# Performance work log

Measured on AMD Instinct MI355X. Metric: run time of the kernel, lower is better.

Reference implementation:

```python
import jax, jax.numpy as jnp
import numpy as np

NUM_NODES = 100000
NUM_RELS = 500
DIM = 64          # input_dim == hidden_dim == output_dim
NUM_EDGES = 1_000_000
LEAKY_SLOPE = 0.01  # torch F.leaky_relu default


def _linear_params(key, fin, fout):
    # torch nn.Linear default init: U(-1/sqrt(fin), 1/sqrt(fin))
    kw, kb = jax.random.split(key)
    s = 1.0 / np.sqrt(fin)
    W = jax.random.uniform(kw, (fout, fin), minval=-s, maxval=s, dtype=jnp.float32)
    b = jax.random.uniform(kb, (fout,), minval=-s, maxval=s, dtype=jnp.float32)
    return W, b


def setup_inputs() -> dict:
    key = jax.random.key(0)
    ks = jax.random.split(key, 12)
    src_idx = jax.random.randint(ks[0], (NUM_EDGES,), 0, NUM_NODES, dtype=jnp.int32)
    dst_idx = jax.random.randint(ks[1], (NUM_EDGES,), 0, NUM_NODES, dtype=jnp.int32)
    rel_idx = jax.random.randint(ks[2], (NUM_EDGES,), 0, NUM_RELS, dtype=jnp.int32)
    ent_embed = jax.random.normal(ks[3], (NUM_NODES, DIM), dtype=jnp.float32)
    rel_embed = jax.random.normal(ks[4], (NUM_RELS, DIM), dtype=jnp.float32)
    W_ent, b_ent = _linear_params(ks[5], DIM, DIM)          # fc_ent
    W_relL, b_relL = _linear_params(ks[6], DIM, DIM)        # fc_rel
    W_rel2, b_rel2 = _linear_params(ks[7], DIM, DIM)        # fc_rel2
    W_rel3, b_rel3 = _linear_params(ks[8], 3 * DIM, DIM)    # fc_rel3
    W_a, b_a = _linear_params(ks[9], DIM, 1)                # a
    W_fc, b_fc = _linear_params(ks[10], 3 * DIM, DIM)       # fc
    return {
        "ent_embed": ent_embed, "rel_embed": rel_embed,
        "W_ent": W_ent, "b_ent": b_ent,
        "W_relL": W_relL, "b_relL": b_relL,
        "W_rel2": W_rel2, "b_rel2": b_rel2,
        "W_rel3": W_rel3, "b_rel3": b_rel3,
        "W_a": W_a, "b_a": b_a,
        "W_fc": W_fc, "b_fc": b_fc,
        "src_idx": src_idx, "dst_idx": dst_idx, "rel_idx": rel_idx,
    }


def reference(ent_embed, rel_embed, W_ent, b_ent, W_relL, b_relL,
              W_rel2, b_rel2, W_rel3, b_rel3, W_a, b_a, W_fc, b_fc,
              src_idx, dst_idx, rel_idx):
    # --- per-edge projections (first=True path: lookup from learned tables) ---
    src = ent_embed[src_idx] @ W_ent.T + b_ent            # [E, D]
    dst = ent_embed[dst_idx] @ W_ent.T + b_ent            # [E, D]
    rel = rel_embed[rel_idx] @ W_relL.T + b_relL          # [E, D]

    # --- edge message c and unnormalized attention b ---
    c = jnp.concatenate([src, dst, rel], axis=1) @ W_fc.T + b_fc   # [E, D]
    logits = jax.nn.leaky_relu((c @ W_a.T + b_a)[:, 0], LEAKY_SLOPE)  # [E]
    b = jnp.exp(logits)                                    # [E] (original uses plain exp)

    # --- scatter-softmax over edges grouped by source node ---
    b_sum = jax.ops.segment_sum(b, src_idx, num_segments=NUM_NODES)  # [N]
    alpha = b / b_sum[src_idx]                             # [E]

    # --- attention-weighted neighbor aggregation ---
    h_ent = jax.ops.segment_sum(alpha[:, None] * c, src_idx,
                                num_segments=NUM_NODES)    # [N, D]

    # --- relation pooling: mean over edges of each relation ---
    rel2 = rel @ W_rel2.T + b_rel2                         # [E, D]
    feats = jnp.concatenate([h_ent[src_idx], h_ent[dst_idx], rel2], axis=1)  # [E, 3D]
    sums = jax.ops.segment_sum(feats, rel_idx, num_segments=NUM_RELS)        # [R, 3D]
    counts = jax.ops.segment_sum(jnp.ones_like(b), rel_idx, num_segments=NUM_RELS)
    mean = sums / jnp.maximum(counts, 1.0)[:, None]        # [R, 3D]

    h_rel = mean @ W_rel3.T + b_rel3                       # [R, D]
    return (h_ent, h_rel)
```

## Files before the change

kernel.cpp:

```cpp
#include <hip/hip_runtime.h>
#include <hip/hip_fp16.h>
#include <math.h>

#define N_NODES 100000
#define N_RELS  500
#define DIM     64
#define N_EDGES 1000000
#define SLOPE   0.01f
#define RSUB    4
#define SC_EDGES 2048
#define NB_E    489
#define NBKT    196
#define BSH     9
#define NROWS   (N_RELS + NBKT)
#define BMAX    5632

__device__ __forceinline__ unsigned short f2bf(float f) {
    unsigned int u = __float_as_uint(f);
    u += 0x7FFFu + ((u >> 16) & 1u);
    return (unsigned short)(u >> 16);
}
__device__ __forceinline__ float bfl(unsigned int u) { return __uint_as_float(u << 16); }
__device__ __forceinline__ float bfh(unsigned int u) { return __uint_as_float(u & 0xFFFF0000u); }

__device__ __forceinline__ unsigned int f2e5m2(float f) {
    __half h = __float2half_rn(f);
    unsigned short hu;
    __builtin_memcpy(&hu, &h, 2);
    unsigned int u = hu;
    u += 0x7Fu + ((u >> 8) & 1u);
    return (u >> 8) & 0xFFu;
}
__device__ __forceinline__ float e5d(unsigned int b) {
    unsigned short u = (unsigned short)(b << 8);
    __half h;
    __builtin_memcpy(&h, &u, 2);
    return __half2float(h);
}
__device__ __forceinline__ void acc8(float* a, unsigned int x, unsigned int y) {
    a[0] += e5d(x & 255u);         a[1] += e5d((x >> 8) & 255u);
    a[2] += e5d((x >> 16) & 255u); a[3] += e5d(x >> 24);
    a[4] += e5d(y & 255u);         a[5] += e5d((y >> 8) & 255u);
    a[6] += e5d((y >> 16) & 255u); a[7] += e5d(y >> 24);
}
__device__ __forceinline__ void acc16(float* a, uint4 w) {
    acc8(a, w.x, w.y);
    acc8(a + 8, w.z, w.w);
}
__device__ __forceinline__ void accvw(float* a, float b, uint4 vv, uint4 ww) {
    a[0] += b * (bfl(vv.x) + bfl(ww.x));
    a[1] += b * (bfh(vv.x) + bfh(ww.x));
    a[2] += b * (bfl(vv.y) + bfl(ww.y));
    a[3] += b * (bfh(vv.y) + bfh(ww.y));
    a[4] += b * (bfl(vv.z) + bfl(ww.z));
    a[5] += b * (bfh(vv.z) + bfh(ww.z));
    a[6] += b * (bfl(vv.w) + bfl(ww.w));
    a[7] += b * (bfh(vv.w) + bfh(ww.w));
}

__global__ void k_fold(const float* __restrict__ W_ent, const float* __restrict__ b_ent,
                       const float* __restrict__ W_relL, const float* __restrict__ b_relL,
                       const float* __restrict__ W_rel2, const float* __restrict__ b_rel2,
                       const float* __restrict__ W_fc, const float* __restrict__ b_fc,
                       float* __restrict__ Wcat, float* __restrict__ dcat,
                       float* __restrict__ MW, float* __restrict__ MQ,
                       float* __restrict__ dW, float* __restrict__ dQ) {
    int idx = blockIdx.x * 256 + threadIdx.x;
    if (idx < 8192) {
        int k = idx >> 7;
        int j2 = idx & 127;
        int jj = j2 & 63;
        int off = (j2 >> 6) * 64;
        float s = 0.f;
        for (int i = 0; i < 64; i++) s += W_fc[jj*192 + off + i] * W_ent[i*64 + k];
        Wcat[k*128 + j2] = s;
    } else if (idx < 12288) {
        int rem = idx - 8192;
        int j = rem >> 6, i = rem & 63;
        float s = 0.f;
        for (int k = 0; k < 64; k++) s += W_fc[j*192 + 128 + k] * W_relL[k*64 + i];
        MW[j*64 + i] = s;
    } else if (idx < 16384) {
        int rem = idx - 12288;
        int j = rem >> 6, i = rem & 63;
        float s = 0.f;
        for (int k = 0; k < 64; k++) s += W_rel2[j*64 + k] * W_relL[k*64 + i];
        MQ[j*64 + i] = s;
    } else if (idx < 16512) {
        int j2 = idx - 16384;
        int jj = j2 & 63;
        int off = (j2 >> 6) * 64;
        float s = 0.f;
        for (int i = 0; i < 64; i++) s += b_ent[i] * W_fc[jj*192 + off + i];
        dcat[j2] = s;
    } else if (idx < 16640) {
        int rem = idx - 16512;
        int vec = rem >> 6, j = rem & 63;
        if (vec == 0) {
            float s = b_fc[j];
            for (int k = 0; k < 64; k++) s += b_relL[k] * W_fc[j*192 + 128 + k];
            dW[j] = s;
        } else {
            float s = b_rel2[j];
            for (int k = 0; k < 64; k++) s += b_relL[k] * W_rel2[j*64 + k];
            dQ[j] = s;
        }
    }
}

__global__ __launch_bounds__(256) void k_node(const float* __restrict__ ent,
        const float* __restrict__ Wcat, const float* __restrict__ dcat,
        const float* __restrict__ W_a,
        float* __restrict__ Uout, unsigned short* __restrict__ V16,
        float* __restrict__ us, float* __restrict__ vs) {
    __shared__ float sA[64][68];
    __shared__ float sW[64][128];
    int t = threadIdx.x;
    int tile0 = blockIdx.x * 64;
    for (int i = t; i < 2048; i += 256)
        ((float4*)sW)[i] = ((const float4*)Wcat)[i];
    for (int f = t; f < 1024; f += 256) {
        int n = f >> 4, k4 = f & 15;
        float4 v4 = (tile0 + n < N_NODES)
            ? ((const float4*)(ent + (size_t)(tile0 + n) * 64))[k4]
            : make_float4(0.f, 0.f, 0.f, 0.f);
        *(float4*)&sA[n][k4 * 4] = v4;
    }
    __syncthreads();

    int ng = t >> 4;
    int jg = t & 15;
    int n0 = ng * 4;
    int j0 = jg * 8;

    float4 d0 = *(const float4*)(dcat + j0);
    float4 d1 = *(const float4*)(dcat + j0 + 4);
    float acc[4][8];
    #pragma unroll
    for (int a = 0; a < 4; a++) {
        acc[a][0] = d0.x; acc[a][1] = d0.y; acc[a][2] = d0.z; acc[a][3] = d0.w;
        acc[a][4] = d1.x; acc[a][5] = d1.y; acc[a][6] = d1.z; acc[a][7] = d1.w;
    }

    #pragma unroll 4
    for (int k = 0; k < 64; k++) {
        float4 w0 = *(const float4*)&sW[k][j0];
        float4 w1 = *(const float4*)&sW[k][j0 + 4];
        float e0 = sA[n0][k], e1 = sA[n0+1][k], e2 = sA[n0+2][k], e3 = sA[n0+3][k];
        float e[4] = {e0, e1, e2, e3};
        #pragma unroll
        for (int a = 0; a < 4; a++) {
            acc[a][0] += e[a] * w0.x; acc[a][1] += e[a] * w0.y;
            acc[a][2] += e[a] * w0.z; acc[a][3] += e[a] * w0.w;
            acc[a][4] += e[a] * w1.x; acc[a][5] += e[a] * w1.y;
            acc[a][6] += e[a] * w1.z; acc[a][7] += e[a] * w1.w;
        }
    }

    int jw = j0 & 63;
    float4 wa0 = *(const float4*)(W_a + jw);
    float4 wa1 = *(const float4*)(W_a + jw + 4);
    float part[4];
    #pragma unroll
    for (int a = 0; a < 4; a++) {
        part[a] = acc[a][0]*wa0.x + acc[a][1]*wa0.y + acc[a][2]*wa0.z + acc[a][3]*wa0.w
                + acc[a][4]*wa1.x + acc[a][5]*wa1.y + acc[a][6]*wa1.z + acc[a][7]*wa1.w;
    }
    #pragma unroll
    for (int m = 1; m <= 4; m <<= 1) {
        #pragma unroll
        for (int a = 0; a < 4; a++) part[a] += __shfl_xor(part[a], m, 64);
    }
    if ((jg & 7) == 0) {
        float* sv = (jg < 8) ? us : vs;
        #pragma unroll
        for (int a = 0; a < 4; a++)
            if (tile0 + n0 + a < N_NODES) sv[tile0 + n0 + a] = part[a];
    }

    #pragma unroll
    for (int a = 0; a < 4; a++) {
        int n = tile0 + n0 + a;
        if (n >= N_NODES) break;
        if (jg < 8) {
            float4 o0 = make_float4(acc[a][0], acc[a][1], acc[a][2], acc[a][3]);
            float4 o1 = make_float4(acc[a][4], acc[a][5], acc[a][6], acc[a][7]);
            float* base = Uout + (size_t)n * 64 + j0;
            *(float4*)(base) = o0;
            *(float4*)(base + 4) = o1;
        } else {
            uint4 pv;
            pv.x = (unsigned int)f2bf(acc[a][0]) | ((unsigned int)f2bf(acc[a][1]) << 16);
            pv.y = (unsigned int)f2bf(acc[a][2]) | ((unsigned int)f2bf(acc[a][3]) << 16);
            pv.z = (unsigned int)f2bf(acc[a][4]) | ((unsigned int)f2bf(acc[a][5]) << 16);
            pv.w = (unsigned int)f2bf(acc[a][6]) | ((unsigned int)f2bf(acc[a][7]) << 16);
            *(uint4*)(V16 + (size_t)n * 64 + (j0 - 64)) = pv;
        }
    }
}

__global__ __launch_bounds__(256, 2) void k_relproj(const float* __restrict__ relE,
        const float* __restrict__ MW, const float* __restrict__ MQ,
        const float* __restrict__ dW, const float* __restrict__ dQ,
        const float* __restrict__ W_a,
        unsigned short* __restrict__ Wr16, float* __restrict__ Qr, float* __restrict__ wsr) {
    int lane = threadIdx.x & 63;
    int wv = threadIdx.x >> 6;
    float mw[64], mq[64];
    #pragma unroll
    for (int i = 0; i < 64; i++) { mw[i] = MW[lane*64 + i]; mq[i] = MQ[lane*64 + i]; }
    float dw = dW[lane], dq = dQ[lane], wa = W_a[lane];
    int r = blockIdx.x * 4 + wv;
    if (r >= N_RELS) return;
    float e = relE[(size_t)r * 64 + lane];
    float w = dw, q = dq;
    #pragma unroll
    for (int i = 0; i < 64; i++) {
        float ei = __shfl(e, i, 64);
        w += ei * mw[i];
        q += ei * mq[i];
    }
    Wr16[(size_t)r * 64 + lane] = f2bf(w);
    Qr[(size_t)r * 64 + lane] = q;
    float tw = w * wa;
    #pragma unroll
    for (int o = 32; o; o >>= 1) tw += __shfl_xor(tw, o, 64);
    if (lane == 0) wsr[r] = tw;
}

__global__ void k_zero(int* __restrict__ a, int n) {
    int g = blockIdx.x * 256 + threadIdx.x;
    if (g < n) a[g] = 0;
}

__global__ __launch_bounds__(256) void k_hist(const int* __restrict__ src, const int* __restrict__ rel,
        int* __restrict__ cnt_rel, int* __restrict__ bucket_cnt, int* __restrict__ blkhist) {
    __shared__ int lcntR[N_RELS];
    __shared__ int lcntS[NBKT];
    int t = threadIdx.x;
    for (int r = t; r < N_RELS; r += 256) lcntR[r] = 0;
    for (int b = t; b < NBKT; b += 256) lcntS[b] = 0;
    __syncthreads();
    int base = blockIdx.x * SC_EDGES;
    if (base + SC_EDGES <= N_EDGES) {
        int e0 = base + t * 8;
        int4 sa = *(const int4*)(src + e0);
        int4 sb = *(const int4*)(src + e0 + 4);
        int4 ra = *(const int4*)(rel + e0);
        int4 rb = *(const int4*)(rel + e0 + 4);
        atomicAdd(&lcntS[sa.x >> BSH], 1); atomicAdd(&lcntS[sa.y >> BSH], 1);
        atomicAdd(&lcntS[sa.z >> BSH], 1); atomicAdd(&lcntS[sa.w >> BSH], 1);
        atomicAdd(&lcntS[sb.x >> BSH], 1); atomicAdd(&lcntS[sb.y >> BSH], 1);
        atomicAdd(&lcntS[sb.z >> BSH], 1); atomicAdd(&lcntS[sb.w >> BSH], 1);
        atomicAdd(&lcntR[ra.x], 1); atomicAdd(&lcntR[ra.y], 1);
        atomicAdd(&lcntR[ra.z], 1); atomicAdd(&lcntR[ra.w], 1);
        atomicAdd(&lcntR[rb.x], 1); atomicAdd(&lcntR[rb.y], 1);
        atomicAdd(&lcntR[rb.z], 1); atomicAdd(&lcntR[rb.w], 1);
    } else {
        for (int g = base + t; g < N_EDGES; g += 256) {
            atomicAdd(&lcntS[src[g] >> BSH], 1);
            atomicAdd(&lcntR[rel[g]], 1);
        }
    }
    __syncthreads();
    for (int r = t; r < N_RELS; r += 256) {
        int c = lcntR[r];
        blkhist[(size_t)r * NB_E + blockIdx.x] = c;
        if (c) atomicAdd(&cnt_rel[r], c);
    }
    for (int b = t; b < NBKT; b += 256) {
        int c = lcntS[b];
        blkhist[(size_t)(N_RELS + b) * NB_E + blockIdx.x] = c;
        if (c) atomicAdd(&bucket_cnt[b], c);
    }
}

__global__ void k_scan_two(const int* __restrict__ cnt_rel, const int* __restrict__ bucket_cnt,
                           int* __restrict__ starts) {
    __shared__ int tot[256];
    int t = threadIdx.x;
    const int* cnt = blockIdx.x ? bucket_cnt : cnt_rel;
    int n = blockIdx.x ? NBKT : N_RELS;
    int* out = starts + (blockIdx.x ? N_RELS : 0);
    int myv[4];
    int mySum = 0;
    for (int q = 0; q < 4; q++) {
        int g = t * 4 + q;
        int v = (g < n) ? cnt[g] : 0;
        myv[q] = v; mySum += v;
    }
    tot[t] = mySum;
    __syncthreads();
    for (int o = 1; o < 256; o <<= 1) {
        int u = (t >= o) ? tot[t - o] : 0;
        __syncthreads();
        tot[t] += u;
        __syncthreads();
    }
    int run = tot[t] - mySum;
    for (int q = 0; q < 4; q++) {
        int g = t * 4 + q;
        if (g < n) out[g] = run;
        run += myv[q];
    }
}

__global__ __launch_bounds__(256) void k_scan_relblk(const int* __restrict__ starts,
        const int* __restrict__ blkhist, int* __restrict__ blkbase) {
    int lane = threadIdx.x & 63;
    int row = (blockIdx.x * 256 + threadIdx.x) >> 6;
    if (row >= NROWS) return;
    int run = starts[row];
    for (int base = 0; base < NB_E; base += 64) {
        int b = base + lane;
        int v = (b < NB_E) ? blkhist[(size_t)row * NB_E + b] : 0;
        int x = v;
        #pragma unroll
        for (int o = 1; o < 64; o <<= 1) {
            int y = __shfl_up(x, o, 64);
            if (lane >= o) x += y;
        }
        if (b < NB_E) blkbase[(size_t)row * NB_E + b] = run + (x - v);
        run += __shfl(x, 63, 64);
    }
}

__global__ __launch_bounds__(256) void k_scatter(const int* __restrict__ src, const int* __restrict__ dst,
        const int* __restrict__ rel, const int* __restrict__ blkbase,
        int2* __restrict__ pay_rel, int* __restrict__ stg_a, int* __restrict__ stg_b) {
    __shared__ int lbaseR[N_RELS];
    __shared__ int loffR[N_RELS];
    __shared__ int lbaseS[NBKT];
    __shared__ int loffS[NBKT];
    int t = threadIdx.x;
    for (int r = t; r < N_RELS; r += 256) {
        lbaseR[r] = blkbase[(size_t)r * NB_E + blockIdx.x];
        loffR[r] = 0;
    }
    for (int b = t; b < NBKT; b += 256) {
        lbaseS[b] = blkbase[(size_t)(N_RELS + b) * NB_E + blockIdx.x];
        loffS[b] = 0;
    }
    __syncthreads();
    int base = blockIdx.x * SC_EDGES;
    if (base + SC_EDGES <= N_EDGES) {
        int e0 = base + t * 8;
        int4 sa = *(const int4*)(src + e0);
        int4 sb = *(const int4*)(src + e0 + 4);
        int4 da = *(const int4*)(dst + e0);
        int4 db = *(const int4*)(dst + e0 + 4);
        int4 ra = *(const int4*)(rel + e0);
        int4 rb = *(const int4*)(rel + e0 + 4);
        int s[8] = {sa.x, sa.y, sa.z, sa.w, sb.x, sb.y, sb.z, sb.w};
        int d[8] = {da.x, da.y, da.z, da.w, db.x, db.y, db.z, db.w};
        int r8[8] = {ra.x, ra.y, ra.z, ra.w, rb.x, rb.y, rb.z, rb.w};
        int p[8], q[8];
        #pragma unroll
        for (int j = 0; j < 8; j++) q[j] = lbaseR[r8[j]] + atomicAdd(&loffR[r8[j]], 1);
        #pragma unroll
        for (int j = 0; j < 8; j++) p[j] = lbaseS[s[j] >> BSH] + atomicAdd(&loffS[s[j] >> BSH], 1);
        #pragma unroll
        for (int j = 0; j < 8; j++) pay_rel[q[j]] = make_int2(s[j], d[j]);
        #pragma unroll
        for (int j = 0; j < 8; j++) stg_a[p[j]] = d[j];
        #pragma unroll
        for (int j = 0; j < 8; j++) stg_b[p[j]] = ((s[j] & 511) << 9) | r8[j];
    } else {
        for (int g = base + t; g < N_EDGES; g += 256) {
            int s = src[g], d = dst[g], r = rel[g];
            int q = lbaseR[r] + atomicAdd(&loffR[r], 1);
            pay_rel[q] = make_int2(s, d);
            int sb2 = s >> BSH;
            int p = lbaseS[sb2] + atomicAdd(&loffS[sb2], 1);
            stg_a[p] = d;
            stg_b[p] = ((s & 511) << 9) | r;
        }
    }
}

__global__ __launch_bounds__(256) void k_sortb(const int* __restrict__ stg_a,
        const int* __restrict__ stg_b, const int* __restrict__ starts,
        const int* __restrict__ bucket_cnt,
        const float* __restrict__ us, const float* __restrict__ vs,
        const float* __restrict__ wsr, const float* __restrict__ b_a_p,
        int2* __restrict__ pay_src, float* __restrict__ pay_b,
        int* __restrict__ start_src, int* __restrict__ cnt_src,
        float* __restrict__ bsum_arr) {
    __shared__ int hist[512];
    __shared__ int lstart[512];
    __shared__ int loff[512];
    __shared__ int tot[256];
    __shared__ float lbsum[512];
    __shared__ int2 lpay[BMAX];
    int bkt = blockIdx.x;
    int base = starts[N_RELS + bkt];
    int n = bucket_cnt[bkt];
    int t = threadIdx.x;
    float ba = b_a_p[0];
    hist[t] = 0; hist[t + 256] = 0;
    lbsum[t] = 0.f; lbsum[t + 256] = 0.f;
    __syncthreads();
    for (int i = t; i < n; i += 256)
        atomicAdd(&hist[stg_b[base + i] >> 9], 1);
    __syncthreads();
    int v0 = hist[t * 2], v1 = hist[t * 2 + 1];
    int mySum = v0 + v1;
    tot[t] = mySum;
    __syncthreads();
    for (int o = 1; o < 256; o <<= 1) {
        int u = (t >= o) ? tot[t - o] : 0;
        __syncthreads();
        tot[t] += u;
        __syncthreads();
    }
    int run = tot[t] - mySum;
    lstart[t * 2] = run;
    lstart[t * 2 + 1] = run + v0;
    loff[t * 2] = 0;
    loff[t * 2 + 1] = 0;
    int node0 = bkt * 512 + t * 2;
    if (node0 < N_NODES) { start_src[node0] = base + run; cnt_src[node0] = v0; }
    if (node0 + 1 < N_NODES) { start_src[node0 + 1] = base + run + v0; cnt_src[node0 + 1] = v1; }
    __syncthreads();
    bool fits = (n <= BMAX);
    for (int i = t; i < n; i += 256) {
        int bb = stg_b[base + i];
        int d = stg_a[base + i];
        int lo = bb >> 9;
        int pos = lstart[lo] + atomicAdd(&loff[lo], 1);
        if (fits) {
            lpay[pos] = make_int2(d, bb);
        } else {
            int r = bb & 511;
            int s = bkt * 512 + lo;
            float t0 = us[s] + vs[d] + wsr[r] + ba;
            t0 = t0 > 0.f ? t0 : SLOPE * t0;
            float b = expf(t0);
            pay_src[base + pos] = make_int2(d, r);
            pay_b[base + pos] = b;
            atomicAdd(&lbsum[lo], b);
        }
    }
    __syncthreads();
    if (fits) {
        for (int i = t; i < n; i += 256) {
            int2 pr = lpay[i];
            int bb = pr.y;
            int lo = bb >> 9;
            int r = bb & 511;
            int s = bkt * 512 + lo;
            float t0 = us[s] + vs[pr.x] + wsr[r] + ba;
            t0 = t0 > 0.f ? t0 : SLOPE * t0;
            float b = expf(t0);
            pay_src[base + i] = make_int2(pr.x, r);
            pay_b[base + i] = b;
            atomicAdd(&lbsum[lo], b);
        }
        __syncthreads();
    }
    if (node0 < N_NODES) bsum_arr[node0] = lbsum[t * 2];
    if (node0 + 1 < N_NODES) bsum_arr[node0 + 1] = lbsum[t * 2 + 1];
}

__global__ __launch_bounds__(256) void k_attn(const int2* __restrict__ pay,
        const float* __restrict__ pay_b,
        const int* __restrict__ start_src, const int* __restrict__ cnt_src,
        const float* __restrict__ bsum_arr,
        const unsigned short* __restrict__ V16, const unsigned short* __restrict__ Wr16,
        float* __restrict__ h, unsigned char* __restrict__ h8) {
    int lane = threadIdx.x & 63;
    int wv = threadIdx.x >> 6;
    int quarter = lane >> 4;
    int lq = lane & 15;
    int slot = lq >> 3;
    int li = lq & 7;
    int n = blockIdx.x * 16 + wv * 4 + quarter;
    if (n >= N_NODES) return;
    int st = start_src[n];
    int cnt = cnt_src[n];
    if (cnt == 0) {
        if (lq < 8) {
            float* hp = h + (size_t)n * 64 + lq * 8;
            *(float4*)hp = make_float4(0.f, 0.f, 0.f, 0.f);
            *(float4*)(hp + 4) = make_float4(0.f, 0.f, 0.f, 0.f);
            *(uint2*)(h8 + (size_t)n * 64 + lq * 8) = make_uint2(0u, 0u);
        }
        return;
    }
    float inv = 1.f / bsum_arr[n];
    float a[8] = {0.f, 0.f, 0.f, 0.f, 0.f, 0.f, 0.f, 0.f};
    for (int e = slot; e < cnt; e += 8) {
        int eB = e + 2, eC = e + 4, eD = e + 6;
        bool vB = eB < cnt, vC = eC < cnt, vD = eD < cnt;
        int cB = vB ? eB : e, cC = vC ? eC : e, cD = vD ? eD : e;
        float bA = pay_b[st + e];
        float bB = vB ? pay_b[st + eB] : 0.f;
        float bC = vC ? pay_b[st + eC] : 0.f;
        float bD = vD ? pay_b[st + eD] : 0.f;
        int2 pA = pay[st + e];
        int2 pB = pay[st + cB];
        int2 pC = pay[st + cC];
        int2 pD = pay[st + cD];
        uint4 vvA = *(const uint4*)(V16 + (size_t)pA.x * 64 + li * 8);
        uint4 wwA = *(const uint4*)(Wr16 + (size_t)pA.y * 64 + li * 8);
        uint4 vvB = *(const uint4*)(V16 + (size_t)pB.x * 64 + li * 8);
        uint4 wwB = *(const uint4*)(Wr16 + (size_t)pB.y * 64 + li * 8);
        uint4 vvC = *(const uint4*)(V16 + (size_t)pC.x * 64 + li * 8);
        uint4 wwC = *(const uint4*)(Wr16 + (size_t)pC.y * 64 + li * 8);
        uint4 vvD = *(const uint4*)(V16 + (size_t)pD.x * 64 + li * 8);
        uint4 wwD = *(const uint4*)(Wr16 + (size_t)pD.y * 64 + li * 8);
        accvw(a, bA, vvA, wwA);
        accvw(a, bB, vvB, wwB);
        accvw(a, bC, vvC, wwC);
        accvw(a, bD, vvD, wwD);
    }
    #pragma unroll
    for (int d = 0; d < 8; d++) a[d] += __shfl_xor(a[d], 8, 64);
    if (slot == 0) {
        float* hp = h + (size_t)n * 64 + li * 8;
        float o[8];
        #pragma unroll
        for (int d = 0; d < 8; d++) o[d] = hp[d] + a[d] * inv;
        *(float4*)hp = make_float4(o[0], o[1], o[2], o[3]);
        *(float4*)(hp + 4) = make_float4(o[4], o[5], o[6], o[7]);
        uint2 p8;
        p8.x = f2e5m2(o[0]) | (f2e5m2(o[1]) << 8) | (f2e5m2(o[2]) << 16) | (f2e5m2(o[3]) << 24);
        p8.y = f2e5m2(o[4]) | (f2e5m2(o[5]) << 8) | (f2e5m2(o[6]) << 16) | (f2e5m2(o[7]) << 24);
        *(uint2*)(h8 + (size_t)n * 64 + lq * 8) = p8;
    }
}

#define RP_STREAMS 8
__global__ __launch_bounds__(256) void k_relpool(const int2* __restrict__ pay,
        const int* __restrict__ start_rel, const int* __restrict__ cnt_rel,
        const unsigned char* __restrict__ h8, float* __restrict__ acc_rel) {
    int r = blockIdx.x / RSUB;
    int sub = blockIdx.x % RSUB;
    int st = start_rel[r];
    int cnt = cnt_rel[r];
    int t = threadIdx.x;
    int li = t & 3;
    int side = (t >> 2) & 1;
    int j = t >> 3;

    int chunk = (cnt + RSUB - 1) / RSUB;
    int k0 = sub * chunk;
    int k1 = min(k0 + chunk, cnt);
    int len = k1 - k0;

    float a[16];
    #pragma unroll
    for (int d = 0; d < 16; d++) a[d] = 0.f;

    if (len > 0) {
        const int2* pp = pay + st + k0;
        int m[RP_STREAMS]; bool v[RP_STREAMS]; int2 p[RP_STREAMS];
        #pragma unroll
        for (int s = 0; s < RP_STREAMS; s++) {
            m[s] = j + s * 32;
            v[s] = m[s] < len;
            p[s] = v[s] ? pp[m[s]] : make_int2(0, 0);
        }
        for (int base = 0; base < len; base += 32 * RP_STREAMS) {
            uint4 hv[RP_STREAMS];
            #pragma unroll
            for (int s = 0; s < RP_STREAMS; s++) {
                int idx = side ? p[s].y : p[s].x;
                hv[s] = *(const uint4*)(h8 + (size_t)idx * 64 + li * 16);
            }
            int mn[RP_STREAMS]; bool vn[RP_STREAMS]; int2 pn[RP_STREAMS];
            #pragma unroll
            for (int s = 0; s < RP_STREAMS; s++) {
                mn[s] = m[s] + 32 * RP_STREAMS;
                vn[s] = mn[s] < len;
                pn[s] = vn[s] ? pp[mn[s]] : make_int2(0, 0);
            }
            #pragma unroll
            for (int s = 0; s < RP_STREAMS; s++) if (v[s]) acc16(a, hv[s]);
            #pragma unroll
            for (int s = 0; s < RP_STREAMS; s++) { m[s] = mn[s]; v[s] = vn[s]; p[s] = pn[s]; }
        }
    }

    #pragma unroll
    for (int d = 0; d < 16; d++) {
        a[d] += __shfl_xor(a[d], 8, 64);
        a[d] += __shfl_xor(a[d], 16, 64);
        a[d] += __shfl_xor(a[d], 32, 64);
    }

    __shared__ float red[4][8][16];
    int wv = t >> 6;
    int lane = t & 63;
    if (lane < 8) {
        #pragma unroll
        for (int d = 0; d < 16; d++) red[wv][lane][d] = a[d];
    }
    __syncthreads();
    if (t < 128) {
        int sl = t >> 4;
        int d = t & 15;
        float s = red[0][sl][d] + red[1][sl][d] + red[2][sl][d] + red[3][sl][d];
        int sd = sl >> 2;
        int li2 = sl & 3;
        atomicAdd(&acc_rel[r * 128 + sd * 64 + li2 * 16 + d], s);
    }
}

__global__ void k_relfin(const float* __restrict__ acc_rel, const int* __restrict__ cnt_rel,
                         const float* __restrict__ Qr, const float* __restrict__ W_rel3,
                         const float* __restrict__ b_rel3, float* __restrict__ out) {
    int g = blockIdx.x * 256 + threadIdx.x;
    if (g >= N_RELS * 64) return;
    int r = g >> 6;
    int j = g & 63;
    int cnt = cnt_rel[r];
    float invc = 1.f / (float)(cnt > 0 ? cnt : 1);
    float s = b_rel3[j];
    for (int k = 0; k < 128; k++) s += acc_rel[r * 128 + k] * invc * W_rel3[j * 192 + k];
    if (cnt > 0)
        for (int k = 0; k < 64; k++) s += Qr[r * 64 + k] * W_rel3[j * 192 + 128 + k];
    out[g] = s;
}

extern "C" void kernel_launch(void* const* d_in, const int* in_sizes, int n_in,
                              void* d_out, int out_size, void* d_ws, size_t ws_size,
                              hipStream_t stream) {
    const float* ent    = (const float*)d_in[0];
    const float* relE   = (const float*)d_in[1];
    const float* W_ent  = (const float*)d_in[2];
    const float* b_ent  = (const float*)d_in[3];
    const float* W_relL = (const float*)d_in[4];
    const float* b_relL = (const float*)d_in[5];
    const float* W_rel2 = (const float*)d_in[6];
    const float* b_rel2 = (const float*)d_in[7];
    const float* W_rel3 = (const float*)d_in[8];
    const float* b_rel3 = (const float*)d_in[9];
    const float* W_a    = (const float*)d_in[10];
    const float* b_a    = (const float*)d_in[11];
    const float* W_fc   = (const float*)d_in[12];
    const float* b_fc   = (const float*)d_in[13];
    const int* src = (const int*)d_in[14];
    const int* dst = (const int*)d_in[15];
    const int* rel = (const int*)d_in[16];
    float* out = (float*)d_out;

    char* ws = (char*)d_ws;
    size_t off = 0;
    auto alloc = [&](size_t bytes) -> void* {
        void* p = ws + off;
        off += (bytes + 255) & ~(size_t)255;
        return p;
    };
    float* Wcat = (float*)alloc(8192 * 4);
    float* dcat = (float*)alloc(128 * 4);
    float* MW  = (float*)alloc(4096 * 4);
    float* MQ  = (float*)alloc(4096 * 4);
    float* dW  = (float*)alloc(64 * 4);
    float* dQ  = (float*)alloc(64 * 4);
    unsigned short* V16 = (unsigned short*)alloc((size_t)N_NODES * 64 * 2);
    unsigned char* h8 = (unsigned char*)alloc((size_t)N_NODES * 64);
    float* us  = (float*)alloc((size_t)N_NODES * 4);
    float* vs  = (float*)alloc((size_t)N_NODES * 4);
    unsigned short* Wr16 = (unsigned short*)alloc((size_t)N_RELS * 64 * 2);
    float* Qr  = (float*)alloc((size_t)N_RELS * 64 * 4);
    float* wsr = (float*)alloc((size_t)N_RELS * 4);
    int* cnt_src   = (int*)alloc((size_t)N_NODES * 4);
    int* start_src = (int*)alloc((size_t)N_NODES * 4);
    float* bsum    = (float*)alloc((size_t)N_NODES * 4);
    int* cnts      = (int*)alloc((size_t)NROWS * 4);
    int* starts    = (int*)alloc((size_t)NROWS * 4);
    int* blkhist   = (int*)alloc((size_t)NROWS * NB_E * 4);
    int* blkbase   = (int*)alloc((size_t)NROWS * NB_E * 4);
    int* stg_a     = (int*)alloc((size_t)N_EDGES * 4);
    int* stg_b     = (int*)alloc((size_t)N_EDGES * 4);
    int2* pay_src  = (int2*)alloc((size_t)N_EDGES * 8);
    float* pay_b   = (float*)alloc((size_t)N_EDGES * 4);
    int2* pay_rel  = (int2*)alloc((size_t)N_EDGES * 8);
    float* acc_rel = (float*)alloc((size_t)N_RELS * 128 * 4);

    int* cnt_rel    = cnts;
    int* bucket_cnt = cnts + N_RELS;

    k_zero<<<(NROWS + 255) / 256, 256, 0, stream>>>(cnts, NROWS);
    k_zero<<<(N_RELS * 128 + 255) / 256, 256, 0, stream>>>((int*)acc_rel, N_RELS * 128);

    k_fold<<<65, 256, 0, stream>>>(W_ent, b_ent, W_relL, b_relL, W_rel2, b_rel2,
                                   W_fc, b_fc, Wcat, dcat, MW, MQ, dW, dQ);
    k_node<<<(N_NODES + 63) / 64, 256, 0, stream>>>(ent, Wcat, dcat, W_a, out, V16, us, vs);
    k_relproj<<<125, 256, 0, stream>>>(relE, MW, MQ, dW, dQ, W_a, Wr16, Qr, wsr);
    k_hist<<<NB_E, 256, 0, stream>>>(src, rel, cnt_rel, bucket_cnt, blkhist);
    k_scan_two<<<2, 256, 0, stream>>>(cnt_rel, bucket_cnt, starts);
    k_scan_relblk<<<(NROWS * 64 + 255) / 256, 256, 0, stream>>>(starts, blkhist, blkbase);
    k_scatter<<<NB_E, 256, 0, stream>>>(src, dst, rel, blkbase, pay_rel, stg_a, stg_b);
    k_sortb<<<NBKT, 256, 0, stream>>>(stg_a, stg_b, starts, bucket_cnt,
                                      us, vs, wsr, b_a,
                                      pay_src, pay_b, start_src, cnt_src, bsum);
    k_attn<<<(N_NODES + 15) / 16, 256, 0, stream>>>(pay_src, pay_b, start_src, cnt_src,
                                                    bsum, V16, Wr16, out, h8);
    k_relpool<<<N_RELS * RSUB, 256, 0, stream>>>(pay_rel, starts, cnt_rel, h8, acc_rel);
    k_relfin<<<(N_RELS * 64 + 255) / 256, 256, 0, stream>>>(acc_rel, cnt_rel, Qr, W_rel3,
                                                            b_rel3, out + (size_t)N_NODES * 64);
}
```

Baseline: 295.0 us.

## Software-pipeline attention gather loop and replace relation atomics with partial buffers

The per-node attention loop now processes two edges per step and prefetches the next step's payload indices and weights (software pipelining), instead of issuing four independent gathers per step. Relation pooling writes per-block partial sums to a buffer that the final kernel reduces, which removes the atomicAdd and the zeroing kernel. The RP_STREAMS constant drops from 8 to 6, and an h8 store index changes from lq to li (equivalent where slot==0). The loop has less memory-level parallelism per iteration, which may hurt latency hiding on the gathers.

```diff
diff --git a/kernel.cpp b/kernel.cpp
--- a/kernel.cpp
+++ b/kernel.cpp
@@ -489,30 +489,32 @@
     }
     float inv = 1.f / bsum_arr[n];
     float a[8] = {0.f, 0.f, 0.f, 0.f, 0.f, 0.f, 0.f, 0.f};
-    for (int e = slot; e < cnt; e += 8) {
-        int eB = e + 2, eC = e + 4, eD = e + 6;
-        bool vB = eB < cnt, vC = eC < cnt, vD = eD < cnt;
-        int cB = vB ? eB : e, cC = vC ? eC : e, cD = vD ? eD : e;
-        float bA = pay_b[st + e];
-        float bB = vB ? pay_b[st + eB] : 0.f;
-        float bC = vC ? pay_b[st + eC] : 0.f;
-        float bD = vD ? pay_b[st + eD] : 0.f;
-        int2 pA = pay[st + e];
-        int2 pB = pay[st + cB];
-        int2 pC = pay[st + cC];
-        int2 pD = pay[st + cD];
+    int eA = slot;
+    int eB = slot + 2;
+    bool vA = eA < cnt;
+    bool vB = eB < cnt;
+    int cA = vA ? eA : 0;
+    int cB = vB ? eB : 0;
+    float bA = vA ? pay_b[st + cA] : 0.f;
+    float bB = vB ? pay_b[st + cB] : 0.f;
+    int2 pA = pay[st + cA];
+    int2 pB = pay[st + cB];
+    while (vA) {
         uint4 vvA = *(const uint4*)(V16 + (size_t)pA.x * 64 + li * 8);
         uint4 wwA = *(const uint4*)(Wr16 + (size_t)pA.y * 64 + li * 8);
         uint4 vvB = *(const uint4*)(V16 + (size_t)pB.x * 64 + li * 8);
         uint4 wwB = *(const uint4*)(Wr16 + (size_t)pB.y * 64 + li * 8);
-        uint4 vvC = *(const uint4*)(V16 + (size_t)pC.x * 64 + li * 8);
-        uint4 wwC = *(const uint4*)(Wr16 + (size_t)pC.y * 64 + li * 8);
-        uint4 vvD = *(const uint4*)(V16 + (size_t)pD.x * 64 + li * 8);
-        uint4 wwD = *(const uint4*)(Wr16 + (size_t)pD.y * 64 + li * 8);
+        int nA = eA + 4, nB = eB + 4;
+        bool wA = nA < cnt, wB = nB < cnt;
+        int dA = wA ? nA : 0, dB = wB ? nB : 0;
+        float nbA = wA ? pay_b[st + dA] : 0.f;
+        float nbB = wB ? pay_b[st + dB] : 0.f;
+        int2 npA = pay[st + dA];
+        int2 npB = pay[st + dB];
         accvw(a, bA, vvA, wwA);
         accvw(a, bB, vvB, wwB);
-        accvw(a, bC, vvC, wwC);
-        accvw(a, bD, vvD, wwD);
+        eA = nA; eB = nB; vA = wA; vB = wB;
+        bA = nbA; bB = nbB; pA = npA; pB = npB;
     }
     #pragma unroll
     for (int d = 0; d < 8; d++) a[d] += __shfl_xor(a[d], 8, 64);
@@ -526,14 +528,14 @@
         uint2 p8;
         p8.x = f2e5m2(o[0]) | (f2e5m2(o[1]) << 8) | (f2e5m2(o[2]) << 16) | (f2e5m2(o[3]) << 24);
         p8.y = f2e5m2(o[4]) | (f2e5m2(o[5]) << 8) | (f2e5m2(o[6]) << 16) | (f2e5m2(o[7]) << 24);
-        *(uint2*)(h8 + (size_t)n * 64 + lq * 8) = p8;
-    }
-}
-
-#define RP_STREAMS 8
+        *(uint2*)(h8 + (size_t)n * 64 + li * 8) = p8;
+    }
+}
+
+#define RP_STREAMS 6
 __global__ __launch_bounds__(256) void k_relpool(const int2* __restrict__ pay,
         const int* __restrict__ start_rel, const int* __restrict__ cnt_rel,
-        const unsigned char* __restrict__ h8, float* __restrict__ acc_rel) {
+        const unsigned char* __restrict__ h8, float* __restrict__ part) {
     int r = blockIdx.x / RSUB;
     int sub = blockIdx.x % RSUB;
     int st = start_rel[r];
@@ -603,11 +605,11 @@
         float s = red[0][sl][d] + red[1][sl][d] + red[2][sl][d] + red[3][sl][d];
         int sd = sl >> 2;
         int li2 = sl & 3;
-        atomicAdd(&acc_rel[r * 128 + sd * 64 + li2 * 16 + d], s);
-    }
-}
-
-__global__ void k_relfin(const float* __restrict__ acc_rel, const int* __restrict__ cnt_rel,
+        part[(size_t)blockIdx.x * 128 + sd * 64 + li2 * 16 + d] = s;
+    }
+}
+
+__global__ void k_relfin(const float* __restrict__ part, const int* __restrict__ cnt_rel,
                          const float* __restrict__ Qr, const float* __restrict__ W_rel3,
                          const float* __restrict__ b_rel3, float* __restrict__ out) {
     int g = blockIdx.x * 256 + threadIdx.x;
@@ -616,8 +618,12 @@
     int j = g & 63;
     int cnt = cnt_rel[r];
     float invc = 1.f / (float)(cnt > 0 ? cnt : 1);
+    const float* p0 = part + (size_t)(r * RSUB) * 128;
     float s = b_rel3[j];
-    for (int k = 0; k < 128; k++) s += acc_rel[r * 128 + k] * invc * W_rel3[j * 192 + k];
+    for (int k = 0; k < 128; k++) {
+        float acc = p0[k] + p0[128 + k] + p0[256 + k] + p0[384 + k];
+        s += acc * invc * W_rel3[j * 192 + k];
+    }
     if (cnt > 0)
         for (int k = 0; k < 64; k++) s += Qr[r * 64 + k] * W_rel3[j * 192 + 128 + k];
     out[g] = s;
@@ -677,13 +683,12 @@
     int2* pay_src  = (int2*)alloc((size_t)N_EDGES * 8);
     float* pay_b   = (float*)alloc((size_t)N_EDGES * 4);
     int2* pay_rel  = (int2*)alloc((size_t)N_EDGES * 8);
-    float* acc_rel = (float*)alloc((size_t)N_RELS * 128 * 4);
+    float* part    = (float*)alloc((size_t)N_RELS * RSUB * 128 * 4);
 
     int* cnt_rel    = cnts;
     int* bucket_cnt = cnts + N_RELS;
 
     k_zero<<<(NROWS + 255) / 256, 256, 0, stream>>>(cnts, NROWS);
-    k_zero<<<(N_RELS * 128 + 255) / 256, 256, 0, stream>>>((int*)acc_rel, N_RELS * 128);
 
     k_fold<<<65, 256, 0, stream>>>(W_ent, b_ent, W_relL, b_relL, W_rel2, b_rel2,
                                    W_fc, b_fc, Wcat, dcat, MW, MQ, dW, dQ);
@@ -698,7 +703,7 @@
                                       pay_src, pay_b, start_src, cnt_src, bsum);
     k_attn<<<(N_NODES + 15) / 16, 256, 0, stream>>>(pay_src, pay_b, start_src, cnt_src,
                                                     bsum, V16, Wr16, out, h8);
-    k_relpool<<<N_RELS * RSUB, 256, 0, stream>>>(pay_rel, starts, cnt_rel, h8, acc_rel);
-    k_relfin<<<(N_RELS * 64 + 255) / 256, 256, 0, stream>>>(acc_rel, cnt_rel, Qr, W_rel3,
+    k_relpool<<<N_RELS * RSUB, 256, 0, stream>>>(pay_rel, starts, cnt_rel, h8, part);
+    k_relfin<<<(N_RELS * 64 + 255) / 256, 256, 0, stream>>>(part, cnt_rel, Qr, W_rel3,
                                                             b_rel3, out + (size_t)N_NODES * 64);
 }
```

Measured after the change: 303.3 us. 1.03x slower.
